# Optimization experiments

Hardware: AMD Instinct MI355X
Metric: run time of the kernel (lower is better)

Reference implementation:

```python
import jax, jax.numpy as jnp
import numpy as np

OUT_F, IN_F, BLOCK, RANK = 8192, 8192, 32, 16
B, S = 4, 256
Q_ZERO = 128.0      # symmetric int8-style zero point for the Q8_0-like quants
LORA_SCALE = 2.0    # patch alpha applied by the patch function


def setup_inputs() -> dict:
    key = jax.random.key(0)
    k1, k2, k3, k4, k5, k6 = jax.random.split(key, 6)
    x = jax.random.normal(k1, (B, S, IN_F), dtype=jnp.float32)
    # block-quantized weight: int quants in [0,256) and per-block scales
    q_int = jax.random.randint(k2, (OUT_F, IN_F // BLOCK, BLOCK), 0, 256, dtype=jnp.int32)
    scales = jax.random.uniform(k3, (OUT_F, IN_F // BLOCK), dtype=jnp.float32) * 0.02
    lora_A = jax.random.normal(k4, (RANK, IN_F), dtype=jnp.float32) * 0.02
    lora_B = jax.random.normal(k5, (OUT_F, RANK), dtype=jnp.float32) * 0.02
    bias = jax.random.normal(k6, (OUT_F,), dtype=jnp.float32)
    return {"x": x, "q_int": q_int, "scales": scales,
            "lora_A": lora_A, "lora_B": lora_B, "bias": bias}


def reference(x, q_int, scales, lora_A, lora_B, bias):
    # --- get_weight(): dequantize GGML block-quantized tensor ---
    # w[o, b, e] = (q[o, b, e] - 128) * scale[o, b]
    w = (q_int.astype(jnp.float32) - Q_ZERO) * scales[:, :, None]   # [out, in//BLOCK, BLOCK]
    w = w.reshape(OUT_F, IN_F)                                      # [out, in]
    # --- apply patch function (LoRA add) ---
    w = w + LORA_SCALE * (lora_B @ lora_A)                          # [out, in]
    # --- cast_bias_weight + F.linear ---
    w = w.astype(x.dtype)
    y = jnp.einsum('bsi,oi->bso', x, w) + bias.astype(x.dtype)      # [B, S, out]
    return y
```

## Files before the change

kernel.cpp:

```cpp
#include <hip/hip_runtime.h>
#include <hip/hip_bf16.h>
#include <stdint.h>

#define OUT_F 8192
#define IN_F  8192
#define RANK  16
#define M_TOT 1024
#define BM 128
#define BN 128
#define BK 64
#define NK (IN_F / BK)
#define SCB (IN_F / 32)

typedef __bf16 bf16x8 __attribute__((ext_vector_type(8)));
typedef float  f32x4  __attribute__((ext_vector_type(4)));

static __device__ __forceinline__ uint32_t pack_bf16(float lo, float hi) {
    uint32_t a = __builtin_bit_cast(uint32_t, lo);
    uint32_t b = __builtin_bit_cast(uint32_t, hi);
    return ((a + 0x8000u) >> 16) | ((b + 0x8000u) & 0xffff0000u);
}

__global__ __launch_bounds__(256) void convert_kernel(
    const float* __restrict__ x, uint2* __restrict__ xb2, float* __restrict__ t)
{
    const int tid = threadIdx.x, b = blockIdx.x;
    if (b < 64) t[b * 256 + tid] = 0.f;
    const float4* x4 = (const float4*)x;
    const int base = b * 256 + tid;
#pragma unroll
    for (int j = 0; j < 8; ++j) {
        const int i = base + j * 262144;
        const float4 v = x4[i];
        uint2 p;
        p.x = pack_bf16(v.x, v.y);
        p.y = pack_bf16(v.z, v.w);
        xb2[i] = p;
    }
}

__global__ __launch_bounds__(256) void lora_t_kernel(
    const float* __restrict__ x, const float* __restrict__ lora_A,
    float* __restrict__ t)
{
    const int b = blockIdx.x;
    const int mt = b >> 4, ks = b & 15;
    const int tid = threadIdx.x, wave = tid >> 6, lane = tid & 63;
    const int fr = lane & 15, quad = lane >> 4;
    const int m = mt * 64 + wave * 16 + fr;
    const int k0 = ks * 512 + quad * 8;

    f32x4 acc = {0.f, 0.f, 0.f, 0.f};
    const float* xr = x + (size_t)m * IN_F + k0;
    const float* ar = lora_A + (size_t)fr * IN_F + k0;

#pragma unroll 4
    for (int s = 0; s < 16; ++s) {
        const float4 x0 = *(const float4*)(xr + s * 32);
        const float4 x1 = *(const float4*)(xr + s * 32 + 4);
        const float4 a0 = *(const float4*)(ar + s * 32);
        const float4 a1 = *(const float4*)(ar + s * 32 + 4);
        bf16x8 af, bfr;
        uint32_t* ap = (uint32_t*)&af;
        uint32_t* bp = (uint32_t*)&bfr;
        ap[0] = pack_bf16(x0.x, x0.y); ap[1] = pack_bf16(x0.z, x0.w);
        ap[2] = pack_bf16(x1.x, x1.y); ap[3] = pack_bf16(x1.z, x1.w);
        bp[0] = pack_bf16(a0.x, a0.y); bp[1] = pack_bf16(a0.z, a0.w);
        bp[2] = pack_bf16(a1.x, a1.y); bp[3] = pack_bf16(a1.z, a1.w);
        acc = __builtin_amdgcn_mfma_f32_16x16x32_bf16(af, bfr, acc, 0, 0, 0);
    }
    const int mout = mt * 64 + wave * 16 + quad * 4;
#pragma unroll
    for (int r = 0; r < 4; ++r)
        atomicAdd(&t[(size_t)(mout + r) * RANK + fr], acc[r]);
}


#define GEMM_STEP(KT, P, CUR, NXT)                                             \
    {                                                                          \
        const int ktn = ((KT) + 2) & (NK - 1);                                 \
        _Pragma("unroll")                                                      \
        for (int j = 0; j < 8; ++j) {                                          \
            const int row = qrow + 16 * j;                                     \
            qv[(P) ^ 1][j] = *(const int4*)(qbase + (size_t)row * IN_F + ktn * BK); \
            sc[(P) ^ 1][j] = scales[(size_t)(n0 + row) * SCB + ktn * 2 + qhi]; \
        }                                                                      \
        const int kta = ((KT) + 1) & (NK - 1);                                 \
        _Pragma("unroll")                                                      \
        for (int i = 0; i < 4; ++i) {                                          \
            __builtin_amdgcn_global_load_lds(                                  \
                (const __attribute__((address_space(1))) uint32_t*)(xsrc + (size_t)kta * BK + (size_t)i * 8 * IN_F), \
                (__attribute__((address_space(3))) uint32_t*)(&xs[NXT][(wave * 32 + i * 8) * BK]), \
                16, 0, 0);                                                     \
        }                                                                      \
        _Pragma("unroll")                                                      \
        for (int j = 0; j < 8; ++j) {                                          \
            const float s = sc[P][j];                                          \
            const float c = -128.f * s;                                        \
            const int4 qq = qv[P][j];                                          \
            uint2 pk;                                                          \
            pk.x = pack_bf16(fmaf((float)qq.x, s, c), fmaf((float)qq.y, s, c)); \
            pk.y = pack_bf16(fmaf((float)qq.z, s, c), fmaf((float)qq.w, s, c)); \
            *(uint2*)(&wt[NXT][(qrow + 16 * j) * BK + wpos]) = pk;             \
        }                                                                      \
        _Pragma("unroll")                                                      \
        for (int kk = 0; kk < BK; kk += 32) {                                  \
            bf16x8 af[4], bfr[4];                                              \
            const int pp = (((kk >> 3) + quad) ^ (fr & 7)) * 8;                \
            _Pragma("unroll")                                                  \
            for (int i = 0; i < 4; ++i)                                        \
                af[i] = *(const bf16x8*)(&xs[CUR][(wm * 64 + i * 16 + fr) * BK + pp]); \
            _Pragma("unroll")                                                  \
            for (int j = 0; j < 4; ++j)                                        \
                bfr[j] = *(const bf16x8*)(&wt[CUR][(wn * 64 + j * 16 + fr) * BK + pp]); \
            _Pragma("unroll")                                                  \
            for (int i = 0; i < 4; ++i)                                        \
                _Pragma("unroll")                                              \
                for (int j = 0; j < 4; ++j)                                    \
                    acc[i][j] = __builtin_amdgcn_mfma_f32_16x16x32_bf16(af[i], bfr[j], acc[i][j], 0, 0, 0); \
        }                                                                      \
        __syncthreads();                                                       \
    }

__global__ __launch_bounds__(256, 2) void gemm_kernel(
    const uint16_t* __restrict__ xb,
    const int*      __restrict__ q,
    const float*    __restrict__ scales,
    const float*    __restrict__ t,
    const float*    __restrict__ loraB,
    const float*    __restrict__ bias,
    float*          __restrict__ out)
{
    __shared__ __align__(16) uint16_t xs[2][BM * BK];
    __shared__ __align__(16) uint16_t wt[2][BN * BK];

    const int bx    = blockIdx.x;
    const int mtile = bx >> 6;
    const int ntile = bx & 63;
    const int m0 = mtile * BM;
    const int n0 = ntile * BN;

    const int tid  = threadIdx.x;
    const int wave = tid >> 6;
    const int lane = tid & 63;
    const int wm = wave & 1, wn = wave >> 1;
    const int fr = lane & 15;
    const int quad = lane >> 4;

    const int qrow  = tid >> 4;
    const int qcol4 = (tid & 15) * 4;
    const int qhi   = (tid >> 3) & 1;
    const int wpos = ((((tid >> 1) & 7) ^ (qrow & 7)) * 8) + (tid & 1) * 4;

    const int* qbase = q + (size_t)n0 * IN_F + qcol4;

    f32x4 acc[4][4];
    const f32x4 z = {0.f, 0.f, 0.f, 0.f};
#pragma unroll
    for (int i = 0; i < 4; ++i)
#pragma unroll
        for (int j = 0; j < 4; ++j) acc[i][j] = z;

    int4  qv[2][8];
    float sc[2][8];

#pragma unroll
    for (int j = 0; j < 8; ++j) {
        const int row = qrow + 16 * j;
        qv[0][j] = *(const int4*)(qbase + (size_t)row * IN_F);
        sc[0][j] = scales[(size_t)(n0 + row) * SCB + qhi];
    }

    {
        if (tid < 128) {
            const int row = tid, s = row & 7;
            const float4* tp = (const float4*)(t + (size_t)(m0 + row) * RANK);
            const float4 v0 = tp[0], v1 = tp[1], v2 = tp[2], v3 = tp[3];
            uint32_t vals[8];
            vals[0] = pack_bf16(v0.x, v0.y); vals[1] = pack_bf16(v0.z, v0.w);
            vals[2] = pack_bf16(v1.x, v1.y); vals[3] = pack_bf16(v1.z, v1.w);
            vals[4] = pack_bf16(v2.x, v2.y); vals[5] = pack_bf16(v2.z, v2.w);
            vals[6] = pack_bf16(v3.x, v3.y); vals[7] = pack_bf16(v3.z, v3.w);
            uint32_t* dst = (uint32_t*)(&xs[0][row * BK]);
#pragma unroll
            for (int c = 0; c < 8; ++c) {
                const int p = (c ^ s) * 4;
                if (c < 2) {
                    dst[p + 0] = vals[c * 4 + 0]; dst[p + 1] = vals[c * 4 + 1];
                    dst[p + 2] = vals[c * 4 + 2]; dst[p + 3] = vals[c * 4 + 3];
                } else {
                    dst[p + 0] = 0; dst[p + 1] = 0; dst[p + 2] = 0; dst[p + 3] = 0;
                }
            }
        } else {
            const int row = tid - 128, s = row & 7;
            const float4* bp = (const float4*)(loraB + (size_t)(n0 + row) * RANK);
            const float4 v0 = bp[0], v1 = bp[1], v2 = bp[2], v3 = bp[3];
            uint32_t vals[8];
            vals[0] = pack_bf16(2.f * v0.x, 2.f * v0.y); vals[1] = pack_bf16(2.f * v0.z, 2.f * v0.w);
            vals[2] = pack_bf16(2.f * v1.x, 2.f * v1.y); vals[3] = pack_bf16(2.f * v1.z, 2.f * v1.w);
            vals[4] = pack_bf16(2.f * v2.x, 2.f * v2.y); vals[5] = pack_bf16(2.f * v2.z, 2.f * v2.w);
            vals[6] = pack_bf16(2.f * v3.x, 2.f * v3.y); vals[7] = pack_bf16(2.f * v3.z, 2.f * v3.w);
            uint32_t* dst = (uint32_t*)(&wt[0][row * BK]);
#pragma unroll
            for (int c = 0; c < 8; ++c) {
                const int p = (c ^ s) * 4;
                if (c < 2) {
                    dst[p + 0] = vals[c * 4 + 0]; dst[p + 1] = vals[c * 4 + 1];
                    dst[p + 2] = vals[c * 4 + 2]; dst[p + 3] = vals[c * 4 + 3];
                } else {
                    dst[p + 0] = 0; dst[p + 1] = 0; dst[p + 2] = 0; dst[p + 3] = 0;
                }
            }
        }
        __syncthreads();
        const int pp = (quad ^ (fr & 7)) * 8;
        bf16x8 af[4], bfr[4];
#pragma unroll
        for (int i = 0; i < 4; ++i)
            af[i] = *(const bf16x8*)(&xs[0][(wm * 64 + i * 16 + fr) * BK + pp]);
#pragma unroll
        for (int j = 0; j < 4; ++j)
            bfr[j] = *(const bf16x8*)(&wt[0][(wn * 64 + j * 16 + fr) * BK + pp]);
#pragma unroll
        for (int i = 0; i < 4; ++i)
#pragma unroll
            for (int j = 0; j < 4; ++j)
                acc[i][j] = __builtin_amdgcn_mfma_f32_16x16x32_bf16(af[i], bfr[j], acc[i][j], 0, 0, 0);
        __syncthreads();
    }

    const int xrow   = wave * 32 + (lane >> 3);
    const int xchunk = (lane & 7) ^ (lane >> 3);
    const uint16_t* xsrc = xb + (size_t)(m0 + xrow) * IN_F + xchunk * 8;

#pragma unroll
    for (int i = 0; i < 4; ++i) {
        __builtin_amdgcn_global_load_lds(
            (const __attribute__((address_space(1))) uint32_t*)(xsrc + (size_t)i * 8 * IN_F),
            (__attribute__((address_space(3))) uint32_t*)(&xs[0][(wave * 32 + i * 8) * BK]),
            16, 0, 0);
    }
#pragma unroll
    for (int j = 0; j < 8; ++j) {
        const float s = sc[0][j];
        const float c = -128.f * s;
        const int4 qq = qv[0][j];
        uint2 pk;
        pk.x = pack_bf16(fmaf((float)qq.x, s, c), fmaf((float)qq.y, s, c));
        pk.y = pack_bf16(fmaf((float)qq.z, s, c), fmaf((float)qq.w, s, c));
        *(uint2*)(&wt[0][(qrow + 16 * j) * BK + wpos]) = pk;
    }
#pragma unroll
    for (int j = 0; j < 8; ++j) {
        const int row = qrow + 16 * j;
        qv[0][j] = *(const int4*)(qbase + (size_t)row * IN_F + 1 * BK);
        sc[0][j] = scales[(size_t)(n0 + row) * SCB + 2 + qhi];
    }
    __syncthreads();

    for (int kt = 0; kt < NK; kt += 2) {
        GEMM_STEP(kt,     0, 0, 1);
        GEMM_STEP(kt + 1, 1, 1, 0);
    }

#pragma unroll
    for (int j = 0; j < 4; ++j) {
        const int col = n0 + wn * 64 + j * 16 + fr;
        const float bv = bias[col];
#pragma unroll
        for (int i = 0; i < 4; ++i) {
            const int rbase = m0 + wm * 64 + i * 16 + quad * 4;
#pragma unroll
            for (int r = 0; r < 4; ++r)
                out[(size_t)(rbase + r) * OUT_F + col] = acc[i][j][r] + bv;
        }
    }
}

extern "C" void kernel_launch(void* const* d_in, const int* in_sizes, int n_in,
                              void* d_out, int out_size, void* d_ws, size_t ws_size,
                              hipStream_t stream) {
    const float* x      = (const float*)d_in[0];
    const int*   q      = (const int*)d_in[1];
    const float* scales = (const float*)d_in[2];
    const float* lora_A = (const float*)d_in[3];
    const float* lora_B = (const float*)d_in[4];
    const float* bias   = (const float*)d_in[5];
    float* out = (float*)d_out;

    uint16_t* xb = (uint16_t*)d_ws;
    float*    t  = (float*)((char*)d_ws + (size_t)M_TOT * IN_F * sizeof(uint16_t));

    convert_kernel<<<M_TOT, 256, 0, stream>>>(x, (uint2*)xb, t);
    lora_t_kernel<<<256, 256, 0, stream>>>(x, lora_A, t);
    gemm_kernel<<<(M_TOT / BM) * (OUT_F / BN), 256, 0, stream>>>(
        xb, q, scales, t, lora_B, bias, out);
}
```

Before: 607.2 us.

## Narrow int32 quants to uint8 in a pre-pass and stream bytes in GEMM

```diff
diff --git a/kernel.cpp b/kernel.cpp
--- a/kernel.cpp
+++ b/kernel.cpp
@@ -37,6 +37,20 @@
         p.y = pack_bf16(v.z, v.w);
         xb2[i] = p;
     }
+}
+
+__global__ __launch_bounds__(256) void narrow_kernel(
+    const int* __restrict__ q, uint8_t* __restrict__ qu8)
+{
+    const size_t base = ((size_t)blockIdx.x * 256 + threadIdx.x) * 16;
+    const int4* src = (const int4*)(q + base);
+    const int4 a = src[0], b = src[1], c = src[2], d = src[3];
+    uint4 o;
+    o.x = (uint32_t)a.x | ((uint32_t)a.y << 8) | ((uint32_t)a.z << 16) | ((uint32_t)a.w << 24);
+    o.y = (uint32_t)b.x | ((uint32_t)b.y << 8) | ((uint32_t)b.z << 16) | ((uint32_t)b.w << 24);
+    o.z = (uint32_t)c.x | ((uint32_t)c.y << 8) | ((uint32_t)c.z << 16) | ((uint32_t)c.w << 24);
+    o.w = (uint32_t)d.x | ((uint32_t)d.y << 8) | ((uint32_t)d.z << 16) | ((uint32_t)d.w << 24);
+    *(uint4*)(qu8 + base) = o;
 }
 
 __global__ __launch_bounds__(256) void lora_t_kernel(
@@ -75,14 +89,13 @@
         atomicAdd(&t[(size_t)(mout + r) * RANK + fr], acc[r]);
 }
 
-
-#define GEMM_STEP(KT, P, CUR, NXT)                                             \
+#define GEMM_STEP_U(KT, P, CUR, NXT)                                           \
     {                                                                          \
         const int ktn = ((KT) + 2) & (NK - 1);                                 \
         _Pragma("unroll")                                                      \
         for (int j = 0; j < 8; ++j) {                                          \
             const int row = qrow + 16 * j;                                     \
-            qv[(P) ^ 1][j] = *(const int4*)(qbase + (size_t)row * IN_F + ktn * BK); \
+            qv[(P) ^ 1][j] = *(const uint32_t*)(qbase + (size_t)row * IN_F + ktn * BK); \
             sc[(P) ^ 1][j] = scales[(size_t)(n0 + row) * SCB + ktn * 2 + qhi]; \
         }                                                                      \
         const int kta = ((KT) + 1) & (NK - 1);                                 \
@@ -97,10 +110,12 @@
         for (int j = 0; j < 8; ++j) {                                          \
             const float s = sc[P][j];                                          \
             const float c = -128.f * s;                                        \
-            const int4 qq = qv[P][j];                                          \
+            const uint32_t qq = qv[P][j];                                      \
             uint2 pk;                                                          \
-            pk.x = pack_bf16(fmaf((float)qq.x, s, c), fmaf((float)qq.y, s, c)); \
-            pk.y = pack_bf16(fmaf((float)qq.z, s, c), fmaf((float)qq.w, s, c)); \
+            pk.x = pack_bf16(fmaf((float)(qq & 0xffu), s, c),                  \
+                             fmaf((float)((qq >> 8) & 0xffu), s, c));          \
+            pk.y = pack_bf16(fmaf((float)((qq >> 16) & 0xffu), s, c),          \
+                             fmaf((float)(qq >> 24), s, c));                   \
             *(uint2*)(&wt[NXT][(qrow + 16 * j) * BK + wpos]) = pk;             \
         }                                                                      \
         _Pragma("unroll")                                                      \
@@ -122,9 +137,9 @@
         __syncthreads();                                                       \
     }
 
-__global__ __launch_bounds__(256, 2) void gemm_kernel(
+__global__ __launch_bounds__(256, 2) void gemm_u8_kernel(
     const uint16_t* __restrict__ xb,
-    const int*      __restrict__ q,
+    const uint8_t*  __restrict__ qu8,
     const float*    __restrict__ scales,
     const float*    __restrict__ t,
     const float*    __restrict__ loraB,
@@ -152,7 +167,7 @@
     const int qhi   = (tid >> 3) & 1;
     const int wpos = ((((tid >> 1) & 7) ^ (qrow & 7)) * 8) + (tid & 1) * 4;
 
-    const int* qbase = q + (size_t)n0 * IN_F + qcol4;
+    const uint8_t* qbase = qu8 + (size_t)n0 * IN_F + qcol4;
 
     f32x4 acc[4][4];
     const f32x4 z = {0.f, 0.f, 0.f, 0.f};
@@ -161,13 +176,13 @@
 #pragma unroll
         for (int j = 0; j < 4; ++j) acc[i][j] = z;
 
-    int4  qv[2][8];
-    float sc[2][8];
+    uint32_t qv[2][8];
+    float    sc[2][8];
 
 #pragma unroll
     for (int j = 0; j < 8; ++j) {
         const int row = qrow + 16 * j;
-        qv[0][j] = *(const int4*)(qbase + (size_t)row * IN_F);
+        qv[0][j] = *(const uint32_t*)(qbase + (size_t)row * IN_F);
         sc[0][j] = scales[(size_t)(n0 + row) * SCB + qhi];
     }
 
@@ -245,6 +260,210 @@
     for (int j = 0; j < 8; ++j) {
         const float s = sc[0][j];
         const float c = -128.f * s;
+        const uint32_t qq = qv[0][j];
+        uint2 pk;
+        pk.x = pack_bf16(fmaf((float)(qq & 0xffu), s, c),
+                         fmaf((float)((qq >> 8) & 0xffu), s, c));
+        pk.y = pack_bf16(fmaf((float)((qq >> 16) & 0xffu), s, c),
+                         fmaf((float)(qq >> 24), s, c));
+        *(uint2*)(&wt[0][(qrow + 16 * j) * BK + wpos]) = pk;
+    }
+#pragma unroll
+    for (int j = 0; j < 8; ++j) {
+        const int row = qrow + 16 * j;
+        qv[0][j] = *(const uint32_t*)(qbase + (size_t)row * IN_F + 1 * BK);
+        sc[0][j] = scales[(size_t)(n0 + row) * SCB + 2 + qhi];
+    }
+    __syncthreads();
+
+    for (int kt = 0; kt < NK; kt += 2) {
+        GEMM_STEP_U(kt,     0, 0, 1);
+        GEMM_STEP_U(kt + 1, 1, 1, 0);
+    }
+
+#pragma unroll
+    for (int j = 0; j < 4; ++j) {
+        const int col = n0 + wn * 64 + j * 16 + fr;
+        const float bv = bias[col];
+#pragma unroll
+        for (int i = 0; i < 4; ++i) {
+            const int rbase = m0 + wm * 64 + i * 16 + quad * 4;
+#pragma unroll
+            for (int r = 0; r < 4; ++r)
+                out[(size_t)(rbase + r) * OUT_F + col] = acc[i][j][r] + bv;
+        }
+    }
+}
+
+#define GEMM_STEP_L(KT, P, CUR, NXT)                                           \
+    {                                                                          \
+        const int ktn = ((KT) + 2) & (NK - 1);                                 \
+        _Pragma("unroll")                                                      \
+        for (int j = 0; j < 8; ++j) {                                          \
+            const int row = qrow + 16 * j;                                     \
+            qv[(P) ^ 1][j] = *(const int4*)(qbase + (size_t)row * IN_F + ktn * BK); \
+            sc[(P) ^ 1][j] = scales[(size_t)(n0 + row) * SCB + ktn * 2 + qhi]; \
+        }                                                                      \
+        const int kta = ((KT) + 1) & (NK - 1);                                 \
+        _Pragma("unroll")                                                      \
+        for (int i = 0; i < 4; ++i) {                                          \
+            __builtin_amdgcn_global_load_lds(                                  \
+                (const __attribute__((address_space(1))) uint32_t*)(xsrc + (size_t)kta * BK + (size_t)i * 8 * IN_F), \
+                (__attribute__((address_space(3))) uint32_t*)(&xs[NXT][(wave * 32 + i * 8) * BK]), \
+                16, 0, 0);                                                     \
+        }                                                                      \
+        _Pragma("unroll")                                                      \
+        for (int j = 0; j < 8; ++j) {                                          \
+            const float s = sc[P][j];                                          \
+            const float c = -128.f * s;                                        \
+            const int4 qq = qv[P][j];                                          \
+            uint2 pk;                                                          \
+            pk.x = pack_bf16(fmaf((float)qq.x, s, c), fmaf((float)qq.y, s, c)); \
+            pk.y = pack_bf16(fmaf((float)qq.z, s, c), fmaf((float)qq.w, s, c)); \
+            *(uint2*)(&wt[NXT][(qrow + 16 * j) * BK + wpos]) = pk;             \
+        }                                                                      \
+        _Pragma("unroll")                                                      \
+        for (int kk = 0; kk < BK; kk += 32) {                                  \
+            bf16x8 af[4], bfr[4];                                              \
+            const int pp = (((kk >> 3) + quad) ^ (fr & 7)) * 8;                \
+            _Pragma("unroll")                                                  \
+            for (int i = 0; i < 4; ++i)                                        \
+                af[i] = *(const bf16x8*)(&xs[CUR][(wm * 64 + i * 16 + fr) * BK + pp]); \
+            _Pragma("unroll")                                                  \
+            for (int j = 0; j < 4; ++j)                                        \
+                bfr[j] = *(const bf16x8*)(&wt[CUR][(wn * 64 + j * 16 + fr) * BK + pp]); \
+            _Pragma("unroll")                                                  \
+            for (int i = 0; i < 4; ++i)                                        \
+                _Pragma("unroll")                                              \
+                for (int j = 0; j < 4; ++j)                                    \
+                    acc[i][j] = __builtin_amdgcn_mfma_f32_16x16x32_bf16(af[i], bfr[j], acc[i][j], 0, 0, 0); \
+        }                                                                      \
+        __syncthreads();                                                       \
+    }
+
+__global__ __launch_bounds__(256, 2) void gemm_kernel(
+    const uint16_t* __restrict__ xb,
+    const int*      __restrict__ q,
+    const float*    __restrict__ scales,
+    const float*    __restrict__ t,
+    const float*    __restrict__ loraB,
+    const float*    __restrict__ bias,
+    float*          __restrict__ out)
+{
+    __shared__ __align__(16) uint16_t xs[2][BM * BK];
+    __shared__ __align__(16) uint16_t wt[2][BN * BK];
+
+    const int bx    = blockIdx.x;
+    const int mtile = bx >> 6;
+    const int ntile = bx & 63;
+    const int m0 = mtile * BM;
+    const int n0 = ntile * BN;
+
+    const int tid  = threadIdx.x;
+    const int wave = tid >> 6;
+    const int lane = tid & 63;
+    const int wm = wave & 1, wn = wave >> 1;
+    const int fr = lane & 15;
+    const int quad = lane >> 4;
+
+    const int qrow  = tid >> 4;
+    const int qcol4 = (tid & 15) * 4;
+    const int qhi   = (tid >> 3) & 1;
+    const int wpos = ((((tid >> 1) & 7) ^ (qrow & 7)) * 8) + (tid & 1) * 4;
+
+    const int* qbase = q + (size_t)n0 * IN_F + qcol4;
+
+    f32x4 acc[4][4];
+    const f32x4 z = {0.f, 0.f, 0.f, 0.f};
+#pragma unroll
+    for (int i = 0; i < 4; ++i)
+#pragma unroll
+        for (int j = 0; j < 4; ++j) acc[i][j] = z;
+
+    int4  qv[2][8];
+    float sc[2][8];
+
+#pragma unroll
+    for (int j = 0; j < 8; ++j) {
+        const int row = qrow + 16 * j;
+        qv[0][j] = *(const int4*)(qbase + (size_t)row * IN_F);
+        sc[0][j] = scales[(size_t)(n0 + row) * SCB + qhi];
+    }
+
+    {
+        if (tid < 128) {
+            const int row = tid, s = row & 7;
+            const float4* tp = (const float4*)(t + (size_t)(m0 + row) * RANK);
+            const float4 v0 = tp[0], v1 = tp[1], v2 = tp[2], v3 = tp[3];
+            uint32_t vals[8];
+            vals[0] = pack_bf16(v0.x, v0.y); vals[1] = pack_bf16(v0.z, v0.w);
+            vals[2] = pack_bf16(v1.x, v1.y); vals[3] = pack_bf16(v1.z, v1.w);
+            vals[4] = pack_bf16(v2.x, v2.y); vals[5] = pack_bf16(v2.z, v2.w);
+            vals[6] = pack_bf16(v3.x, v3.y); vals[7] = pack_bf16(v3.z, v3.w);
+            uint32_t* dst = (uint32_t*)(&xs[0][row * BK]);
+#pragma unroll
+            for (int c = 0; c < 8; ++c) {
+                const int p = (c ^ s) * 4;
+                if (c < 2) {
+                    dst[p + 0] = vals[c * 4 + 0]; dst[p + 1] = vals[c * 4 + 1];
+                    dst[p + 2] = vals[c * 4 + 2]; dst[p + 3] = vals[c * 4 + 3];
+                } else {
+                    dst[p + 0] = 0; dst[p + 1] = 0; dst[p + 2] = 0; dst[p + 3] = 0;
+                }
+            }
+        } else {
+            const int row = tid - 128, s = row & 7;
+            const float4* bp = (const float4*)(loraB + (size_t)(n0 + row) * RANK);
+            const float4 v0 = bp[0], v1 = bp[1], v2 = bp[2], v3 = bp[3];
+            uint32_t vals[8];
+            vals[0] = pack_bf16(2.f * v0.x, 2.f * v0.y); vals[1] = pack_bf16(2.f * v0.z, 2.f * v0.w);
+            vals[2] = pack_bf16(2.f * v1.x, 2.f * v1.y); vals[3] = pack_bf16(2.f * v1.z, 2.f * v1.w);
+            vals[4] = pack_bf16(2.f * v2.x, 2.f * v2.y); vals[5] = pack_bf16(2.f * v2.z, 2.f * v2.w);
+            vals[6] = pack_bf16(2.f * v3.x, 2.f * v3.y); vals[7] = pack_bf16(2.f * v3.z, 2.f * v3.w);
+            uint32_t* dst = (uint32_t*)(&wt[0][row * BK]);
+#pragma unroll
+            for (int c = 0; c < 8; ++c) {
+                const int p = (c ^ s) * 4;
+                if (c < 2) {
+                    dst[p + 0] = vals[c * 4 + 0]; dst[p + 1] = vals[c * 4 + 1];
+                    dst[p + 2] = vals[c * 4 + 2]; dst[p + 3] = vals[c * 4 + 3];
+                } else {
+                    dst[p + 0] = 0; dst[p + 1] = 0; dst[p + 2] = 0; dst[p + 3] = 0;
+                }
+            }
+        }
+        __syncthreads();
+        const int pp = (quad ^ (fr & 7)) * 8;
+        bf16x8 af[4], bfr[4];
+#pragma unroll
+        for (int i = 0; i < 4; ++i)
+            af[i] = *(const bf16x8*)(&xs[0][(wm * 64 + i * 16 + fr) * BK + pp]);
+#pragma unroll
+        for (int j = 0; j < 4; ++j)
+            bfr[j] = *(const bf16x8*)(&wt[0][(wn * 64 + j * 16 + fr) * BK + pp]);
+#pragma unroll
+        for (int i = 0; i < 4; ++i)
+#pragma unroll
+            for (int j = 0; j < 4; ++j)
+                acc[i][j] = __builtin_amdgcn_mfma_f32_16x16x32_bf16(af[i], bfr[j], acc[i][j], 0, 0, 0);
+        __syncthreads();
+    }
+
+    const int xrow   = wave * 32 + (lane >> 3);
+    const int xchunk = (lane & 7) ^ (lane >> 3);
+    const uint16_t* xsrc = xb + (size_t)(m0 + xrow) * IN_F + xchunk * 8;
+
+#pragma unroll
+    for (int i = 0; i < 4; ++i) {
+        __builtin_amdgcn_global_load_lds(
+            (const __attribute__((address_space(1))) uint32_t*)(xsrc + (size_t)i * 8 * IN_F),
+            (__attribute__((address_space(3))) uint32_t*)(&xs[0][(wave * 32 + i * 8) * BK]),
+            16, 0, 0);
+    }
+#pragma unroll
+    for (int j = 0; j < 8; ++j) {
+        const float s = sc[0][j];
+        const float c = -128.f * s;
         const int4 qq = qv[0][j];
         uint2 pk;
         pk.x = pack_bf16(fmaf((float)qq.x, s, c), fmaf((float)qq.y, s, c));
@@ -260,8 +479,8 @@
     __syncthreads();
 
     for (int kt = 0; kt < NK; kt += 2) {
-        GEMM_STEP(kt,     0, 0, 1);
-        GEMM_STEP(kt + 1, 1, 1, 0);
+        GEMM_STEP_L(kt,     0, 0, 1);
+        GEMM_STEP_L(kt + 1, 1, 1, 0);
     }
 
 #pragma unroll
@@ -289,11 +508,25 @@
     const float* bias   = (const float*)d_in[5];
     float* out = (float*)d_out;
 
+    const size_t xb_bytes = (size_t)M_TOT * IN_F * sizeof(uint16_t);
+    const size_t t_bytes  = (size_t)M_TOT * RANK * sizeof(float);
+    const size_t q8_off   = xb_bytes + t_bytes;
+    const size_t q8_bytes = (size_t)OUT_F * IN_F;
+
     uint16_t* xb = (uint16_t*)d_ws;
-    float*    t  = (float*)((char*)d_ws + (size_t)M_TOT * IN_F * sizeof(uint16_t));
-
-    convert_kernel<<<M_TOT, 256, 0, stream>>>(x, (uint2*)xb, t);
-    lora_t_kernel<<<256, 256, 0, stream>>>(x, lora_A, t);
-    gemm_kernel<<<(M_TOT / BM) * (OUT_F / BN), 256, 0, stream>>>(
-        xb, q, scales, t, lora_B, bias, out);
-}
+    float*    t  = (float*)((char*)d_ws + xb_bytes);
+
+    if (ws_size >= q8_off + q8_bytes) {
+        uint8_t* qu8 = (uint8_t*)d_ws + q8_off;
+        narrow_kernel<<<(OUT_F / 256) * (IN_F / 16), 256, 0, stream>>>(q, qu8);
+        convert_kernel<<<M_TOT, 256, 0, stream>>>(x, (uint2*)xb, t);
+        lora_t_kernel<<<256, 256, 0, stream>>>(x, lora_A, t);
+        gemm_u8_kernel<<<(M_TOT / BM) * (OUT_F / BN), 256, 0, stream>>>(
+            xb, qu8, scales, t, lora_B, bias, out);
+    } else {
+        convert_kernel<<<M_TOT, 256, 0, stream>>>(x, (uint2*)xb, t);
+        lora_t_kernel<<<256, 256, 0, stream>>>(x, lora_A, t);
+        gemm_kernel<<<(M_TOT / BM) * (OUT_F / BN), 256, 0, stream>>>(
+            xb, q, scales, t, lora_B, bias, out);
+    }
+}
```

Measured after the change: 607.2 us. About the same (+0.0%).
